# Performance work log

Measured on AMD Instinct MI355X. Metric: run time of the kernel, lower is better.

The kernel has to match this reference:

```python
import jax, jax.numpy as jnp
import numpy as np

B, E, CIN, O = 2, 50000, 8, 128


def _mesh_conv(x, gemm, w, b):
    # MeshCNN MeshConv: x (B,C,E), gemm (B,E,4) neighbor indices, w (O,C,5), b (O,)
    # gather 4 GeMM neighbors per edge, build 5 symmetric features, 1x5 conv
    neigh = jax.vmap(lambda xb, gb: xb[:, gb])(x, gemm)  # (B,C,E,4)
    f1, f2, f3, f4 = neigh[..., 0], neigh[..., 1], neigh[..., 2], neigh[..., 3]
    G = jnp.stack([x, f1 + f3, f2 + f4, jnp.abs(f1 - f3), jnp.abs(f2 - f4)], axis=-1)  # (B,C,E,5)
    return jnp.einsum('bces,ocs->boe', G, w) + b[None, :, None]


def _inorm(x, eps=1e-5):
    # InstanceNorm (no affine, biased variance) over the edge dim, per (batch, channel)
    m = jnp.mean(x, axis=-1, keepdims=True)
    v = jnp.var(x, axis=-1, keepdims=True)
    return (x - m) * jax.lax.rsqrt(v + eps)


def _conv1(x, w, b):
    # 1x1 Conv1d: x (B,C,E), w (O,C)
    return jnp.einsum('bce,oc->boe', x, w) + b[None, :, None]


def setup_inputs() -> dict:
    key = jax.random.key(0)
    ks = jax.random.split(key, 16)

    def W(k, shape, fan):
        return jax.random.normal(k, shape, jnp.float32) * np.float32(1.0 / np.sqrt(fan))

    d = {}
    d['fe'] = jax.random.normal(ks[0], (B, CIN, E), jnp.float32)
    d['gemm'] = jax.random.randint(ks[1], (B, E, 4), 0, E)
    # first-stage MeshConvs: geometry branch (5 ch) and position branch (3 ch)
    d['w_e1'] = W(ks[2], (O, 5, 5), 25);       d['b_e1'] = jnp.zeros((O,), jnp.float32)
    d['w_p1'] = W(ks[3], (O, 3, 5), 15);       d['b_p1'] = jnp.zeros((O,), jnp.float32)
    # residual-block MeshConvs (blocks=1)
    d['w_e2'] = W(ks[4], (O, O, 5), O * 5);    d['b_e2'] = jnp.zeros((O,), jnp.float32)
    d['w_p2'] = W(ks[5], (O, O, 5), O * 5);    d['b_p2'] = jnp.zeros((O,), jnp.float32)
    # Attn(in_dim=O)
    d['wa'] = W(ks[6], (O // 4, O), O);        d['ba'] = jnp.zeros((O // 4,), jnp.float32)
    d['wb'] = W(ks[7], (O // 4, O), O);        d['bb'] = jnp.zeros((O // 4,), jnp.float32)
    d['wal'] = W(ks[8], (O // 2, O // 2), O // 2);  d['bal'] = jnp.zeros((O // 2,), jnp.float32)
    d['wbl'] = W(ks[9], (O // 2, O // 2), O // 2);  d['bbl'] = jnp.zeros((O // 2,), jnp.float32)
    d['wat'] = W(ks[10], (O // 2, O // 2, 5), O // 2 * 5); d['bat'] = jnp.zeros((O // 2,), jnp.float32)
    d['wbt'] = W(ks[11], (O // 2, O // 2, 5), O // 2 * 5); d['bbt'] = jnp.zeros((O // 2,), jnp.float32)
    d['waf'] = W(ks[12], (O, O), O);           d['baf'] = jnp.zeros((O,), jnp.float32)
    d['wbf'] = W(ks[13], (O, O), O);           d['bbf'] = jnp.zeros((O,), jnp.float32)
    return d


def reference(fe, gemm, w_e1, b_e1, w_p1, b_p1, w_e2, b_e2, w_p2, b_p2,
              wa, ba, wb, bb, wal, bal, wbl, bbl, wat, bat, wbt, bbt,
              waf, baf, wbf, bbf):
    # DownConv (8-channel input path): split into edge (5) and point (3) branches
    fe_e, fe_p = fe[:, :5, :], fe[:, 5:, :]
    x1_e = jax.nn.relu(_inorm(_mesh_conv(fe_e, gemm, w_e1, b_e1)))
    x2_e = jax.nn.relu(_inorm(_mesh_conv(x1_e, gemm, w_e2, b_e2)) + x1_e)
    x1_p = jax.nn.relu(_inorm(_mesh_conv(fe_p, gemm, w_p1, b_p1)))
    x2_p = jax.nn.relu(_inorm(_mesh_conv(x1_p, gemm, w_p2, b_p2)) + x1_p)
    # Attn fusion
    x_all = jnp.concatenate([_conv1(x2_e, wa, ba), _conv1(x2_p, wb, bb)], axis=1)  # (B, O/2, E)
    x_a_two = jnp.concatenate([_conv1(x_all, wal, bal), _mesh_conv(x_all, gemm, wat, bat)], axis=1)
    x_b_two = jnp.concatenate([_conv1(x_all, wbl, bbl), _mesh_conv(x_all, gemm, wbt, bbt)], axis=1)
    wA = jax.nn.sigmoid(_inorm(_conv1(x_a_two, waf, baf)))  # (B,O,E)
    wB = jax.nn.sigmoid(_inorm(_conv1(x_b_two, wbf, bbf)))
    weights = jax.nn.softmax(jnp.stack([wA, wB], axis=1), axis=1)  # (B,2,O,E)
    agg = x2_e * weights[:, 0] + x2_p * weights[:, 1]
    # x2_ep = cat(x2_e, x2_p); also emit the attention-fused combine (before_pool)
    return jnp.concatenate([x2_e, x2_p, agg], axis=1)  # (B, 3*O, E)
```

## Files before the change

kernel.cpp:

```cpp
#include <hip/hip_runtime.h>
#include <cstdio>
#include <math.h>


#define E_TOT 50000
#define B_TOT 2
#define TILE_E 64
#define NBLK ((E_TOT + TILE_E - 1) / TILE_E)

typedef _Float16 half_t;
typedef __attribute__((ext_vector_type(4))) _Float16 h4;
typedef __attribute__((ext_vector_type(8))) _Float16 h8;
typedef __attribute__((ext_vector_type(4))) float f32x4;

__device__ __forceinline__ float sigmoidf_(float x) {
    return 1.0f / (1.0f + __expf(-x));
}
__device__ __forceinline__ h8 habs8(h8 x) {
    union { h8 h; unsigned int u[4]; } v;
    v.h = x;
#pragma unroll
    for (int i = 0; i < 4; ++i) v.u[i] &= 0x7FFF7FFFu;
    return v.h;
}

#define OFF_W1E   0
#define OFF_W1P   8192
#define OFF_WTE2  16384
#define OFF_WTP2  98304
#define OFF_WHA   180224
#define OFF_WHB   221184
#define OFF_WTA   262144
#define OFF_WTB   266240
#define OFF_WTAF  270336
#define OFF_WTBF  286720
#define WARENA_N  303104

__global__ __launch_bounds__(256)
void wprep_k(half_t* __restrict__ wa_,
             const float* __restrict__ w_e1, const float* __restrict__ w_p1,
             const float* __restrict__ w_e2, const float* __restrict__ w_p2,
             const float* __restrict__ wat,  const float* __restrict__ wbt,
             const float* __restrict__ wa,   const float* __restrict__ wb,
             const float* __restrict__ wal,  const float* __restrict__ wbl,
             const float* __restrict__ waf,  const float* __restrict__ wbf)
{
    int idx = blockIdx.x * 256 + threadIdx.x;
    switch (blockIdx.y) {
    case 0: if (idx < 8192) { int o = idx >> 6, k = idx & 63, s = k >> 3, cc = k & 7;
            float v = (s < 5 && cc < 5) ? w_e1[o * 25 + cc * 5 + s] : 0.f;
            wa_[OFF_W1E + idx] = (half_t)v; } break;
    case 1: if (idx < 8192) { int o = idx >> 6, k = idx & 63, s = k >> 3, cc = k & 7;
            float v = (s < 5 && cc >= 5) ? w_p1[o * 15 + (cc - 5) * 5 + s] : 0.f;
            wa_[OFF_W1P + idx] = (half_t)v; } break;
    case 2: if (idx < 81920) { int o = idx / 640, r = idx % 640, s = r >> 7, c = r & 127;
            wa_[OFF_WTE2 + idx] = (half_t)w_e2[(o * 128 + c) * 5 + s]; } break;
    case 3: if (idx < 81920) { int o = idx / 640, r = idx % 640, s = r >> 7, c = r & 127;
            wa_[OFF_WTP2 + idx] = (half_t)w_p2[(o * 128 + c) * 5 + s]; } break;
    case 4: if (idx < 40960) { int o = idx / 320, r = idx % 320, s = r >> 6, c = r & 63;
            float v = (o < 64) ? (s == 0 ? wal[o * 64 + c] : 0.f)
                               : wat[((o - 64) * 64 + c) * 5 + s];
            wa_[OFF_WHA + idx] = (half_t)v; } break;
    case 5: if (idx < 40960) { int o = idx / 320, r = idx % 320, s = r >> 6, c = r & 63;
            float v = (o < 64) ? (s == 0 ? wbl[o * 64 + c] : 0.f)
                               : wbt[((o - 64) * 64 + c) * 5 + s];
            wa_[OFF_WHB + idx] = (half_t)v; } break;
    case 6: if (idx < 4096)  wa_[OFF_WTA  + idx] = (half_t)wa[idx];  break;
    case 7: if (idx < 4096)  wa_[OFF_WTB  + idx] = (half_t)wb[idx];  break;
    case 8: if (idx < 16384) wa_[OFF_WTAF + idx] = (half_t)waf[idx]; break;
    case 9: if (idx < 16384) wa_[OFF_WTBF + idx] = (half_t)wbf[idx]; break;
    }
}

__global__ __launch_bounds__(256)
void transpose_in_k(const float* __restrict__ fe, float* __restrict__ fet)
{
    int b = blockIdx.z;
    int e = blockIdx.x * 256 + threadIdx.x;
    if (e >= E_TOT) return;
    float v[8];
#pragma unroll
    for (int c = 0; c < 8; ++c)
        v[c] = fe[((long)b * 8 + c) * E_TOT + e];
    float4* dst = (float4*)&fet[((long)b * E_TOT + e) * 8];
    dst[0] = make_float4(v[0], v[1], v[2], v[3]);
    dst[1] = make_float4(v[4], v[5], v[6], v[7]);
}

__global__ __launch_bounds__(512)
void mesh1_both_k(const float* __restrict__ fet, const int* __restrict__ gemm,
                  const half_t* __restrict__ war,
                  const float* __restrict__ be1, const float* __restrict__ bp1,
                  half_t* __restrict__ tmpe, half_t* __restrict__ tmpp,
                  float* __restrict__ parte, float* __restrict__ partp)
{
    __shared__ h8 Gl[64 * 8];
    __shared__ int nidx[64][4];

    const int tid  = threadIdx.x;
    const int b    = blockIdx.y;
    const int e0   = blockIdx.x * TILE_E;
    const int lane = tid & 63;
    const int wv   = tid >> 6;
    const int l15  = lane & 15;
    const int kg   = lane >> 4;
    const int br   = wv >> 2;
    const int o0   = (wv & 3) * 32;

    const float* xb = fet + (long)b * E_TOT * 8;

    if (tid < 256) {
        int e = tid >> 2, s = tid & 3;
        int eg = e0 + e;
        nidx[e][s] = (eg < E_TOT) ? gemm[((long)b * E_TOT + eg) * 4 + s] : 0;
    }
    __syncthreads();

    {
        int e = tid >> 3, g = tid & 7;
        int eg = e0 + e;
        int se = (eg < E_TOT) ? eg : 0;
        h8 r;
        if (g == 0) {
            const float* p = xb + (long)se * 8;
            float4 v0 = *(const float4*)p, v1 = *(const float4*)(p + 4);
            r[0] = (half_t)v0.x; r[1] = (half_t)v0.y; r[2] = (half_t)v0.z; r[3] = (half_t)v0.w;
            r[4] = (half_t)v1.x; r[5] = (half_t)v1.y; r[6] = (half_t)v1.z; r[7] = (half_t)v1.w;
        } else if (g <= 4) {
            int ia = (g == 1 || g == 3) ? 0 : 1;
            const float* pa = xb + (long)nidx[e][ia] * 8;
            const float* pb = xb + (long)nidx[e][ia + 2] * 8;
            float4 a0 = *(const float4*)pa, a1 = *(const float4*)(pa + 4);
            float4 b0 = *(const float4*)pb, b1 = *(const float4*)(pb + 4);
            float aa[8] = {a0.x, a0.y, a0.z, a0.w, a1.x, a1.y, a1.z, a1.w};
            float bb[8] = {b0.x, b0.y, b0.z, b0.w, b1.x, b1.y, b1.z, b1.w};
            if (g <= 2) {
#pragma unroll
                for (int j = 0; j < 8; ++j) r[j] = (half_t)(aa[j] + bb[j]);
            } else {
#pragma unroll
                for (int j = 0; j < 8; ++j) r[j] = (half_t)fabsf(aa[j] - bb[j]);
            }
        } else {
#pragma unroll
            for (int j = 0; j < 8; ++j) r[j] = (half_t)0.f;
        }
        Gl[(e * 8 + g) ^ (e & 7)] = r;
    }
    __syncthreads();

    f32x4 acc[4][2];
#pragma unroll
    for (int mt = 0; mt < 4; ++mt)
#pragma unroll
        for (int nt = 0; nt < 2; ++nt)
#pragma unroll
            for (int j = 0; j < 4; ++j) acc[mt][nt][j] = 0.f;

    const half_t* wt = war + (br ? OFF_W1P : OFF_W1E);
#pragma unroll
    for (int ks = 0; ks < 2; ++ks) {
        h8 bw[2];
#pragma unroll
        for (int nt = 0; nt < 2; ++nt)
            bw[nt] = *(const h8*)(wt + (long)(o0 + nt * 16 + l15) * 64 + ks * 32 + kg * 8);
#pragma unroll
        for (int mt = 0; mt < 4; ++mt) {
            int row = mt * 16 + l15;
            h8 a = Gl[row * 8 + ((ks * 4 + kg) ^ (row & 7))];
#pragma unroll
            for (int nt = 0; nt < 2; ++nt)
                acc[mt][nt] = __builtin_amdgcn_mfma_f32_16x16x32_f16(a, bw[nt], acc[mt][nt], 0, 0, 0);
        }
    }

    const float* bias = br ? bp1 : be1;
    half_t* yb = (br ? tmpp : tmpe) + (long)b * E_TOT * 128;
    float* part = br ? partp : parte;
    float bv[2], s1[2], s2[2];
#pragma unroll
    for (int nt = 0; nt < 2; ++nt) {
        bv[nt] = bias[o0 + nt * 16 + l15];
        s1[nt] = 0.f; s2[nt] = 0.f;
    }
#pragma unroll
    for (int mt = 0; mt < 4; ++mt) {
        int ebase = e0 + mt * 16 + (kg << 2);
#pragma unroll
        for (int j = 0; j < 4; ++j) {
            if (ebase + j < E_TOT) {
#pragma unroll
                for (int nt = 0; nt < 2; ++nt) {
                    float v = acc[mt][nt][j] + bv[nt];
                    yb[(long)(ebase + j) * 128 + o0 + nt * 16 + l15] = (half_t)v;
                    s1[nt] += v; s2[nt] += v * v;
                }
            }
        }
    }
#pragma unroll
    for (int nt = 0; nt < 2; ++nt) {
        s1[nt] += __shfl_xor(s1[nt], 16); s1[nt] += __shfl_xor(s1[nt], 32);
        s2[nt] += __shfl_xor(s2[nt], 16); s2[nt] += __shfl_xor(s2[nt], 32);
    }
    if (lane < 16) {
        long pb = ((long)b * NBLK + blockIdx.x) * 128;
#pragma unroll
        for (int nt = 0; nt < 2; ++nt) {
            part[(pb + o0 + nt * 16 + lane) * 2 + 0] = s1[nt];
            part[(pb + o0 + nt * 16 + lane) * 2 + 1] = s2[nt];
        }
    }
}

__global__ __launch_bounds__(512, 4)
void mesh2i_k(const half_t* __restrict__ x1i, const int* __restrict__ gemm,
              const half_t* __restrict__ war,
              const float* __restrict__ be, const float* __restrict__ bp,
              half_t* __restrict__ tmpe, half_t* __restrict__ tmpp,
              float* __restrict__ parte, float* __restrict__ partp)
{
    __shared__ h8 B0[1024], B1[1024], B2[1024], B3[1024];
    __shared__ int nidx[64][4];

    const int tid  = threadIdx.x;
    const int b    = blockIdx.y;
    const int e0   = blockIdx.x * TILE_E;
    const int lane = tid & 63;
    const int wv   = tid >> 6;
    const int br   = wv >> 2;
    const int o0   = (wv & 3) * 32;
    const int l15  = lane & 15;
    const int kg   = lane >> 4;

    const half_t* xb = x1i + (long)b * E_TOT * 256;

    if (tid < 256) {
        int e = tid >> 2, s = tid & 3;
        int eg = e0 + e;
        nidx[e][s] = (eg < E_TOT) ? gemm[((long)b * E_TOT + eg) * 4 + s] : 0;
    }
    __syncthreads();

    int te[4], tc[4], tslot[4];
#pragma unroll
    for (int t = 0; t < 4; ++t) {
        int q = t * 512 + tid;
        te[t] = q >> 5; tc[t] = q & 31;
        tslot[t] = (te[t] * 16 + (tc[t] & 15)) ^ (te[t] & 7);
    }

#pragma unroll
    for (int t = 0; t < 4; ++t) {
        int eg = e0 + te[t];
        int se = (eg < E_TOT) ? eg : 0;
        h8 v = *(const h8*)(xb + (long)se * 256 + tc[t] * 8);
        ((tc[t] >> 4) ? B1 : B0)[tslot[t]] = v;
    }
    h8 rA[4], rB[4];
#pragma unroll
    for (int t = 0; t < 4; ++t) {
        int na = nidx[te[t]][0], nb = nidx[te[t]][2];
        rA[t] = *(const h8*)(xb + (long)na * 256 + tc[t] * 8);
        rB[t] = *(const h8*)(xb + (long)nb * 256 + tc[t] * 8);
    }
    __syncthreads();

    f32x4 acc[4][2];
#pragma unroll
    for (int mt = 0; mt < 4; ++mt)
#pragma unroll
        for (int nt = 0; nt < 2; ++nt)
#pragma unroll
            for (int j = 0; j < 4; ++j) acc[mt][nt][j] = 0.f;

    const half_t* wt = war + (br ? OFF_WTP2 : OFF_WTE2);
    auto chunk = [&](const h8* bufE, const h8* bufP, int s) {
        const h8* buf = br ? bufP : bufE;
#pragma unroll
        for (int ks = 0; ks < 4; ++ks) {
            h8 bw0 = *(const h8*)(wt + ((long)(o0 + l15) * 5 + s) * 128 + ks * 32 + kg * 8);
            h8 bw1 = *(const h8*)(wt + ((long)(o0 + 16 + l15) * 5 + s) * 128 + ks * 32 + kg * 8);
#pragma unroll
            for (int mt = 0; mt < 4; ++mt) {
                int row = mt * 16 + l15;
                h8 a = buf[row * 16 + ((ks * 4 + kg) ^ (row & 7))];
                acc[mt][0] = __builtin_amdgcn_mfma_f32_16x16x32_f16(a, bw0, acc[mt][0], 0, 0, 0);
                acc[mt][1] = __builtin_amdgcn_mfma_f32_16x16x32_f16(a, bw1, acc[mt][1], 0, 0, 0);
            }
        }
    };

    chunk(B0, B1, 0);
    __syncthreads();

#pragma unroll
    for (int t = 0; t < 4; ++t) {
        h8 sv = rA[t] + rB[t];
        h8 dv = habs8(rA[t] - rB[t]);
        if (tc[t] >> 4) { B3[tslot[t]] = sv; B1[tslot[t]] = dv; }
        else            { B2[tslot[t]] = sv; B0[tslot[t]] = dv; }
    }
#pragma unroll
    for (int t = 0; t < 4; ++t) {
        int na = nidx[te[t]][1], nb = nidx[te[t]][3];
        rA[t] = *(const h8*)(xb + (long)na * 256 + tc[t] * 8);
        rB[t] = *(const h8*)(xb + (long)nb * 256 + tc[t] * 8);
    }
    __syncthreads();

    chunk(B2, B3, 1);
    chunk(B0, B1, 3);
    __syncthreads();

#pragma unroll
    for (int t = 0; t < 4; ++t) {
        h8 sv = rA[t] + rB[t];
        h8 dv = habs8(rA[t] - rB[t]);
        if (tc[t] >> 4) { B3[tslot[t]] = sv; B1[tslot[t]] = dv; }
        else            { B2[tslot[t]] = sv; B0[tslot[t]] = dv; }
    }
    __syncthreads();

    chunk(B2, B3, 2);
    chunk(B0, B1, 4);

    const float* bias = br ? bp : be;
    half_t* yb = (br ? tmpp : tmpe) + (long)b * E_TOT * 128;
    float* part = br ? partp : parte;
    float bv0 = bias[o0 + l15], bv1 = bias[o0 + 16 + l15];
    float s1a = 0.f, s2a = 0.f, s1b = 0.f, s2b = 0.f;
#pragma unroll
    for (int mt = 0; mt < 4; ++mt) {
        int ebase = e0 + mt * 16 + (kg << 2);
#pragma unroll
        for (int j = 0; j < 4; ++j) {
            if (ebase + j < E_TOT) {
                float v0 = acc[mt][0][j] + bv0;
                float v1 = acc[mt][1][j] + bv1;
                yb[(long)(ebase + j) * 128 + o0 + l15]      = (half_t)v0;
                yb[(long)(ebase + j) * 128 + o0 + 16 + l15] = (half_t)v1;
                s1a += v0; s2a += v0 * v0;
                s1b += v1; s2b += v1 * v1;
            }
        }
    }
    s1a += __shfl_xor(s1a, 16); s1a += __shfl_xor(s1a, 32);
    s2a += __shfl_xor(s2a, 16); s2a += __shfl_xor(s2a, 32);
    s1b += __shfl_xor(s1b, 16); s1b += __shfl_xor(s1b, 32);
    s2b += __shfl_xor(s2b, 16); s2b += __shfl_xor(s2b, 32);
    if (lane < 16) {
        long pb = ((long)b * NBLK + blockIdx.x) * 128;
        part[(pb + o0 + lane) * 2 + 0]      = s1a;
        part[(pb + o0 + lane) * 2 + 1]      = s2a;
        part[(pb + o0 + 16 + lane) * 2 + 0] = s1b;
        part[(pb + o0 + 16 + lane) * 2 + 1] = s2b;
    }
}

__global__ __launch_bounds__(512, 4)
void heads2_k(const half_t* __restrict__ xall, const int* __restrict__ gemm,
              const half_t* __restrict__ war,
              const float* __restrict__ bal, const float* __restrict__ bbl,
              const float* __restrict__ bat, const float* __restrict__ bbt,
              half_t* __restrict__ xa2, half_t* __restrict__ xb2)
{
    __shared__ h8 C0[512], C1[512], C2[512];
    __shared__ int nidx[64][4];

    const int tid  = threadIdx.x;
    const int b    = blockIdx.y;
    const int e0   = blockIdx.x * TILE_E;
    const int lane = tid & 63;
    const int wv   = tid >> 6;
    const int hd   = wv >> 2;
    const int o0   = (wv & 3) * 32;
    const int l15  = lane & 15;
    const int kg   = lane >> 4;

    const half_t* xb = xall + (long)b * E_TOT * 64;

    if (tid < 256) {
        int e = tid >> 2, s = tid & 3;
        int eg = e0 + e;
        nidx[e][s] = (eg < E_TOT) ? gemm[((long)b * E_TOT + eg) * 4 + s] : 0;
    }
    __syncthreads();

    const int te = tid >> 3, tc = tid & 7;
    const int tslot = (te * 8 + tc) ^ (te & 7);

    {
        int eg = e0 + te;
        int se = (eg < E_TOT) ? eg : 0;
        C0[tslot] = *(const h8*)(xb + (long)se * 64 + tc * 8);
    }
    h8 rA, rB;
    {
        int na = nidx[te][0], nb = nidx[te][2];
        rA = *(const h8*)(xb + (long)na * 64 + tc * 8);
        rB = *(const h8*)(xb + (long)nb * 64 + tc * 8);
    }
    __syncthreads();

    f32x4 acc[4][2];
#pragma unroll
    for (int mt = 0; mt < 4; ++mt)
#pragma unroll
        for (int nt = 0; nt < 2; ++nt)
#pragma unroll
            for (int j = 0; j < 4; ++j) acc[mt][nt][j] = 0.f;

    const half_t* wt = war + (hd ? OFF_WHB : OFF_WHA);
    auto chunk = [&](const h8* buf, int s) {
#pragma unroll
        for (int ks = 0; ks < 2; ++ks) {
            h8 bw0 = *(const h8*)(wt + ((long)(o0 + l15) * 5 + s) * 64 + ks * 32 + kg * 8);
            h8 bw1 = *(const h8*)(wt + ((long)(o0 + 16 + l15) * 5 + s) * 64 + ks * 32 + kg * 8);
#pragma unroll
            for (int mt = 0; mt < 4; ++mt) {
                int row = mt * 16 + l15;
                h8 a = buf[row * 8 + ((ks * 4 + kg) ^ (row & 7))];
                acc[mt][0] = __builtin_amdgcn_mfma_f32_16x16x32_f16(a, bw0, acc[mt][0], 0, 0, 0);
                acc[mt][1] = __builtin_amdgcn_mfma_f32_16x16x32_f16(a, bw1, acc[mt][1], 0, 0, 0);
            }
        }
    };

    chunk(C0, 0);
    __syncthreads();
    {
        C1[tslot] = rA + rB;
        C2[tslot] = habs8(rA - rB);
        int na = nidx[te][1], nb = nidx[te][3];
        rA = *(const h8*)(xb + (long)na * 64 + tc * 8);
        rB = *(const h8*)(xb + (long)nb * 64 + tc * 8);
    }
    __syncthreads();
    chunk(C1, 1);
    chunk(C2, 3);
    __syncthreads();
    {
        C1[tslot] = rA + rB;
        C2[tslot] = habs8(rA - rB);
    }
    __syncthreads();
    chunk(C1, 2);
    chunk(C2, 4);

    half_t* yb = (hd ? xb2 : xa2) + (long)b * E_TOT * 128;
    float bv[2];
#pragma unroll
    for (int nt = 0; nt < 2; ++nt) {
        int o = o0 + nt * 16 + l15;
        bv[nt] = (o < 64) ? (hd ? bbl[o] : bal[o]) : (hd ? bbt[o - 64] : bat[o - 64]);
    }
#pragma unroll
    for (int mt = 0; mt < 4; ++mt) {
        int ebase = e0 + mt * 16 + (kg << 2);
#pragma unroll
        for (int j = 0; j < 4; ++j) {
            if (ebase + j < E_TOT) {
#pragma unroll
                for (int nt = 0; nt < 2; ++nt)
                    yb[(long)(ebase + j) * 128 + o0 + nt * 16 + l15] =
                        (half_t)(acc[mt][nt][j] + bv[nt]);
            }
        }
    }
}

__global__ __launch_bounds__(512)
void gates_k(const half_t* __restrict__ xa2, const half_t* __restrict__ xb2,
             const half_t* __restrict__ war,
             const float* __restrict__ baf, const float* __restrict__ bbf,
             half_t* __restrict__ tmpe, half_t* __restrict__ tmpp,
             float* __restrict__ parte, float* __restrict__ partp)
{
    __shared__ h8 Gl[64 * 16];

    const int tid  = threadIdx.x;
    const int br   = blockIdx.y;
    const int b    = blockIdx.z;
    const int e0   = blockIdx.x * TILE_E;
    const int lane = tid & 63;
    const int wv   = tid >> 6;
    const int l15  = lane & 15;
    const int kg   = lane >> 4;
    const int o0   = wv * 16;

    const half_t* xb = (br ? xb2 : xa2) + (long)b * E_TOT * 128;
    const half_t* wt = war + (br ? OFF_WTBF : OFF_WTAF);

#pragma unroll
    for (int t = 0; t < 2; ++t) {
        int q = t * 512 + tid;
        int e = q >> 4, c8 = q & 15;
        int eg = e0 + e;
        int se = (eg < E_TOT) ? eg : 0;
        Gl[(e * 16 + c8) ^ (e & 7)] = *(const h8*)(xb + (long)se * 128 + c8 * 8);
    }
    __syncthreads();

    f32x4 acc[4];
#pragma unroll
    for (int mt = 0; mt < 4; ++mt)
#pragma unroll
        for (int j = 0; j < 4; ++j) acc[mt][j] = 0.f;

#pragma unroll
    for (int ks = 0; ks < 4; ++ks) {
        h8 bw = *(const h8*)(wt + (long)(o0 + l15) * 128 + ks * 32 + kg * 8);
#pragma unroll
        for (int mt = 0; mt < 4; ++mt) {
            int row = mt * 16 + l15;
            h8 a = Gl[row * 16 + ((ks * 4 + kg) ^ (row & 7))];
            acc[mt] = __builtin_amdgcn_mfma_f32_16x16x32_f16(a, bw, acc[mt], 0, 0, 0);
        }
    }

    const float* bias = br ? bbf : baf;
    half_t* yb = (br ? tmpp : tmpe) + (long)b * E_TOT * 128;
    float* part = br ? partp : parte;
    float bv = bias[o0 + l15];
    float s1 = 0.f, s2 = 0.f;
#pragma unroll
    for (int mt = 0; mt < 4; ++mt) {
        int ebase = e0 + mt * 16 + (kg << 2);
#pragma unroll
        for (int j = 0; j < 4; ++j) {
            if (ebase + j < E_TOT) {
                float v = acc[mt][j] + bv;
                yb[(long)(ebase + j) * 128 + o0 + l15] = (half_t)v;
                s1 += v; s2 += v * v;
            }
        }
    }
    s1 += __shfl_xor(s1, 16); s1 += __shfl_xor(s1, 32);
    s2 += __shfl_xor(s2, 16); s2 += __shfl_xor(s2, 32);
    if (lane < 16) {
        long pb = ((long)b * NBLK + blockIdx.x) * 128;
        part[(pb + o0 + lane) * 2 + 0] = s1;
        part[(pb + o0 + lane) * 2 + 1] = s2;
    }
}

__global__ __launch_bounds__(256)
void xall_k(const half_t* __restrict__ x2e, const half_t* __restrict__ x2p,
            const half_t* __restrict__ war,
            const float* __restrict__ ba, const float* __restrict__ bb,
            half_t* __restrict__ xall)
{
    __shared__ h8 Gl[64 * 16];

    const int tid  = threadIdx.x;
    const int br   = blockIdx.y;
    const int b    = blockIdx.z;
    const int e0   = blockIdx.x * TILE_E;
    const int lane = tid & 63;
    const int wv   = tid >> 6;
    const int l15  = lane & 15;
    const int kg   = lane >> 4;
    const int eoff = wv * 16;

    const half_t* xb = (br ? x2p : x2e) + (long)b * E_TOT * 128;
    const half_t* wt = war + (br ? OFF_WTB : OFF_WTA);

#pragma unroll
    for (int t = 0; t < 4; ++t) {
        int q = t * 256 + tid;
        int e = q >> 4, c8 = q & 15;
        int eg = e0 + e;
        int se = (eg < E_TOT) ? eg : 0;
        Gl[(e * 16 + c8) ^ (e & 7)] = *(const h8*)(xb + (long)se * 128 + c8 * 8);
    }
    __syncthreads();

    f32x4 acc[2];
#pragma unroll
    for (int nt = 0; nt < 2; ++nt)
#pragma unroll
        for (int j = 0; j < 4; ++j) acc[nt][j] = 0.f;

#pragma unroll
    for (int ks = 0; ks < 4; ++ks) {
        h8 bw[2];
#pragma unroll
        for (int nt = 0; nt < 2; ++nt)
            bw[nt] = *(const h8*)(wt + (long)(nt * 16 + l15) * 128 + ks * 32 + kg * 8);
        int row = eoff + l15;
        h8 a = Gl[row * 16 + ((ks * 4 + kg) ^ (row & 7))];
#pragma unroll
        for (int nt = 0; nt < 2; ++nt)
            acc[nt] = __builtin_amdgcn_mfma_f32_16x16x32_f16(a, bw[nt], acc[nt], 0, 0, 0);
    }

    const float* bias = br ? bb : ba;
    half_t* yb = xall + (long)b * E_TOT * 64;
    int oOff = br * 32;
#pragma unroll
    for (int nt = 0; nt < 2; ++nt) {
        float bv = bias[nt * 16 + l15];
        int ebase = e0 + eoff + (kg << 2);
#pragma unroll
        for (int j = 0; j < 4; ++j) {
            if (ebase + j < E_TOT)
                yb[(long)(ebase + j) * 64 + oOff + nt * 16 + l15] = (half_t)(acc[nt][j] + bv);
        }
    }
}

__global__ __launch_bounds__(256)
void stats2_k(const float* __restrict__ parte, const float* __restrict__ partp,
              float* __restrict__ statse, float* __restrict__ statsp)
{
    int g = blockIdx.x;
    int br = g >> 8, rem = g & 255, b = rem >> 7, o = rem & 127;
    const float* part = br ? partp : parte;
    float* stats = br ? statsp : statse;
    int tid = threadIdx.x;
    float s1 = 0.f, s2 = 0.f;
    for (int k = tid; k < NBLK; k += 256) {
        long base = (((long)b * NBLK + k) * 128 + o) * 2;
        s1 += part[base];
        s2 += part[base + 1];
    }
#pragma unroll
    for (int d = 1; d < 64; d <<= 1) {
        s1 += __shfl_xor(s1, d);
        s2 += __shfl_xor(s2, d);
    }
    __shared__ float r1[4], r2[4];
    int wv = tid >> 6;
    if ((tid & 63) == 0) { r1[wv] = s1; r2[wv] = s2; }
    __syncthreads();
    if (tid == 0) {
        s1 = r1[0] + r1[1] + r1[2] + r1[3];
        s2 = r2[0] + r2[1] + r2[2] + r2[3];
        float mean = s1 / (float)E_TOT;
        float var  = s2 / (float)E_TOT - mean * mean;
        var = fmaxf(var, 0.f);
        stats[(b * 128 + o) * 2 + 0] = mean;
        stats[(b * 128 + o) * 2 + 1] = rsqrtf(var + 1e-5f);
    }
}

__global__ __launch_bounds__(256)
void norm_act2_k(const half_t* __restrict__ tmpe, const half_t* __restrict__ tmpp,
                 const float* __restrict__ statse, const float* __restrict__ statsp,
                 half_t* __restrict__ x1i)
{
    const long PER = (long)B_TOT * E_TOT * 16;
    long q = (long)blockIdx.x * 256 + threadIdx.x;
    if (q >= 2 * PER) return;
    int br = (q >= PER);
    q -= (long)br * PER;
    const half_t* src = br ? tmpp : tmpe;
    const float* stats = br ? statsp : statse;
    long idx = q * 8;
    int c = (int)(idx & 127);
    long be = idx >> 7;
    int b = (int)(be / E_TOT);
    int e = (int)(be % E_TOT);
    h8 v = *(const h8*)&src[idx];
    h8 r;
#pragma unroll
    for (int j = 0; j < 8; ++j) {
        float2 st = *(const float2*)&stats[(b * 128 + c + j) * 2];
        float t = ((float)v[j] - st.x) * st.y;
        r[j] = (half_t)fmaxf(t, 0.f);
    }
    *(h8*)&x1i[((long)b * E_TOT + e) * 256 + br * 128 + c] = r;
}

__global__ __launch_bounds__(256)
void normres2_k(const half_t* __restrict__ tmpe, const half_t* __restrict__ tmpp,
                const half_t* __restrict__ x1i,
                const float* __restrict__ statse, const float* __restrict__ statsp,
                float* __restrict__ outb,
                half_t* __restrict__ x2e, half_t* __restrict__ x2p)
{
    __shared__ float T[32 * 68];
    int br = blockIdx.y >> 2, cg = blockIdx.y & 3;
    int b = blockIdx.z;
    int e0 = blockIdx.x * 64;
    int tid = threadIdx.x;
    const half_t* xin = br ? tmpp : tmpe;
    const float* stats = br ? statsp : statse;
    half_t* x2b = br ? x2p : x2e;
    int sect = br * 128;
#pragma unroll
    for (int i = 0; i < 2; ++i) {
        int q = tid + i * 256;
        int e = q >> 3, cq = q & 7;
        int eg = e0 + e;
        int se = (eg < E_TOT) ? eg : (E_TOT - 1);
        int c = cg * 32 + cq * 4;
        long base = ((long)b * E_TOT + se) * 128 + c;
        h4 v4 = *(const h4*)&xin[base];
        h4 r4 = *(const h4*)&x1i[((long)b * E_TOT + se) * 256 + br * 128 + c];
        h4 o4;
#pragma unroll
        for (int j = 0; j < 4; ++j) {
            float2 st = *(const float2*)&stats[(b * 128 + c + j) * 2];
            float t = ((float)v4[j] - st.x) * st.y + (float)r4[j];
            t = fmaxf(t, 0.f);
            T[(cq * 4 + j) * 68 + e] = t;
            o4[j] = (half_t)t;
        }
        if (eg < E_TOT) *(h4*)&x2b[base] = o4;
    }
    __syncthreads();
#pragma unroll
    for (int i = 0; i < 2; ++i) {
        int q = tid + i * 256;
        int cl = q >> 4, eq = q & 15;
        int e4 = e0 + eq * 4;
        int cglob = sect + cg * 32 + cl;
        float4 v = *(const float4*)&T[cl * 68 + eq * 4];
        long obase = ((long)b * 384 + cglob) * E_TOT + e4;
        if (e4 + 3 < E_TOT) {
            *(float4*)&outb[obase] = v;
        } else {
            const float* vp = &v.x;
            for (int j = 0; j < 4; ++j)
                if (e4 + j < E_TOT) outb[obase + j] = vp[j];
        }
    }
}

__global__ __launch_bounds__(256)
void gate_agg2_k(const half_t* __restrict__ tA, const half_t* __restrict__ tB,
                 const float* __restrict__ statsA, const float* __restrict__ statsB,
                 const half_t* __restrict__ x2e, const half_t* __restrict__ x2p,
                 float* __restrict__ outb)
{
    __shared__ float T[32 * 68];
    int b = blockIdx.z, cg = blockIdx.y;
    int e0 = blockIdx.x * 64;
    int tid = threadIdx.x;
#pragma unroll
    for (int i = 0; i < 2; ++i) {
        int q = tid + i * 256;
        int e = q >> 3, cq = q & 7;
        int eg = e0 + e;
        int se = (eg < E_TOT) ? eg : (E_TOT - 1);
        int c = cg * 32 + cq * 4;
        long base = ((long)b * E_TOT + se) * 128 + c;
        h4 a4 = *(const h4*)&tA[base];
        h4 b4 = *(const h4*)&tB[base];
        h4 xe4 = *(const h4*)&x2e[base];
        h4 xp4 = *(const h4*)&x2p[base];
#pragma unroll
        for (int j = 0; j < 4; ++j) {
            float2 sa = *(const float2*)&statsA[(b * 128 + c + j) * 2];
            float2 sb = *(const float2*)&statsB[(b * 128 + c + j) * 2];
            float na = sigmoidf_(((float)a4[j] - sa.x) * sa.y);
            float nb = sigmoidf_(((float)b4[j] - sb.x) * sb.y);
            float s = sigmoidf_(na - nb);
            T[(cq * 4 + j) * 68 + e] = (float)xe4[j] * s + (float)xp4[j] * (1.f - s);
        }
    }
    __syncthreads();
#pragma unroll
    for (int i = 0; i < 2; ++i) {
        int q = tid + i * 256;
        int cl = q >> 4, eq = q & 15;
        int e4 = e0 + eq * 4;
        int cglob = cg * 32 + cl;
        float4 v = *(const float4*)&T[cl * 68 + eq * 4];
        long ab = ((long)b * 384 + 256 + cglob) * E_TOT + e4;
        if (e4 + 3 < E_TOT) {
            *(float4*)&outb[ab] = v;
        } else {
            const float* vp = &v.x;
            for (int j = 0; j < 4; ++j)
                if (e4 + j < E_TOT) outb[ab + j] = vp[j];
        }
    }
}

extern "C" void kernel_launch(void* const* d_in, const int* in_sizes, int n_in,
                              void* d_out, int out_size, void* d_ws, size_t ws_size,
                              hipStream_t stream)
{
    const float* fe   = (const float*)d_in[0];
    const int*   gemm = (const int*)  d_in[1];
    const float* w_e1 = (const float*)d_in[2];  const float* b_e1 = (const float*)d_in[3];
    const float* w_p1 = (const float*)d_in[4];  const float* b_p1 = (const float*)d_in[5];
    const float* w_e2 = (const float*)d_in[6];  const float* b_e2 = (const float*)d_in[7];
    const float* w_p2 = (const float*)d_in[8];  const float* b_p2 = (const float*)d_in[9];
    const float* wa   = (const float*)d_in[10]; const float* ba   = (const float*)d_in[11];
    const float* wb   = (const float*)d_in[12]; const float* bb   = (const float*)d_in[13];
    const float* wal  = (const float*)d_in[14]; const float* bal  = (const float*)d_in[15];
    const float* wbl  = (const float*)d_in[16]; const float* bbl  = (const float*)d_in[17];
    const float* wat  = (const float*)d_in[18]; const float* bat  = (const float*)d_in[19];
    const float* wbt  = (const float*)d_in[20]; const float* bbt  = (const float*)d_in[21];
    const float* waf  = (const float*)d_in[22]; const float* baf  = (const float*)d_in[23];
    const float* wbf  = (const float*)d_in[24]; const float* bbf  = (const float*)d_in[25];
    float* out = (float*)d_out;

    const long EB = (long)E_TOT;

    char* wp = (char*)d_ws;
    auto alloc = [&](size_t bytes) -> void* {
        void* r = (void*)wp;
        wp += (bytes + 255) & ~(size_t)255;
        return r;
    };
    float*  FET    = (float*)alloc((size_t)B_TOT * EB * 8 * 4);
    half_t* TMP_E  = (half_t*)alloc((size_t)B_TOT * EB * 128 * 2);
    half_t* TMP_P  = (half_t*)alloc((size_t)B_TOT * EB * 128 * 2);
    half_t* X1I    = (half_t*)alloc((size_t)B_TOT * EB * 256 * 2);
    half_t* X2E    = (half_t*)alloc((size_t)B_TOT * EB * 128 * 2);
    half_t* X2P    = (half_t*)alloc((size_t)B_TOT * EB * 128 * 2);
    half_t* XALL   = (half_t*)alloc((size_t)B_TOT * EB * 64 * 2);
    float*  PART_E = (float*)alloc((size_t)B_TOT * NBLK * 128 * 2 * 4);
    float*  PART_P = (float*)alloc((size_t)B_TOT * NBLK * 128 * 2 * 4);
    float*  STATSE = (float*)alloc((size_t)B_TOT * 128 * 2 * 4);
    float*  STATSP = (float*)alloc((size_t)B_TOT * 128 * 2 * 4);
    half_t* WAR    = (half_t*)alloc((size_t)WARENA_N * 2);

    if ((size_t)(wp - (char*)d_ws) > ws_size) {
        fprintf(stderr, "kernel_launch: ws too small (%zu < %zu)\n",
                ws_size, (size_t)(wp - (char*)d_ws));
        return;
    }

    half_t* XA2 = X1I;
    half_t* XB2 = X1I + (size_t)B_TOT * EB * 128;

    dim3 blk256(256), blk512(512);
    dim3 gI(NBLK, B_TOT);
    dim3 gE2(NBLK, 2, B_TOT);
    dim3 gT((E_TOT + 255) / 256, 1, B_TOT);
    dim3 gN8(NBLK, 8, B_TOT);
    dim3 gN4(NBLK, 4, B_TOT);
    int gA2 = (int)((2 * (long)B_TOT * EB * 16 + 255) / 256);

    wprep_k<<<dim3(320, 10, 1), blk256, 0, stream>>>(WAR,
        w_e1, w_p1, w_e2, w_p2, wat, wbt, wa, wb, wal, wbl, waf, wbf);
    transpose_in_k<<<gT, blk256, 0, stream>>>(fe, FET);

    mesh1_both_k<<<gI, blk512, 0, stream>>>(FET, gemm, WAR, b_e1, b_p1,
        TMP_E, TMP_P, PART_E, PART_P);
    stats2_k<<<512, blk256, 0, stream>>>(PART_E, PART_P, STATSE, STATSP);
    norm_act2_k<<<gA2, blk256, 0, stream>>>(TMP_E, TMP_P, STATSE, STATSP, X1I);

    mesh2i_k<<<gI, blk512, 0, stream>>>(X1I, gemm, WAR, b_e2, b_p2,
        TMP_E, TMP_P, PART_E, PART_P);
    stats2_k<<<512, blk256, 0, stream>>>(PART_E, PART_P, STATSE, STATSP);
    normres2_k<<<gN8, blk256, 0, stream>>>(TMP_E, TMP_P, X1I, STATSE, STATSP,
        out, X2E, X2P);

    xall_k<<<gE2, blk256, 0, stream>>>(X2E, X2P, WAR, ba, bb, XALL);

    heads2_k<<<gI, blk512, 0, stream>>>(XALL, gemm, WAR, bal, bbl, bat, bbt, XA2, XB2);

    gates_k<<<gE2, blk512, 0, stream>>>(XA2, XB2, WAR, baf, bbf,
        TMP_E, TMP_P, PART_E, PART_P);
    stats2_k<<<512, blk256, 0, stream>>>(PART_E, PART_P, STATSE, STATSP);
    gate_agg2_k<<<gN4, blk256, 0, stream>>>(TMP_E, TMP_P, STATSE, STATSP,
        X2E, X2P, out);
}
```

Before: 375.7 us.

## Split interleaved X1 buffer and run branch-separate mesh conv blocks

Replaces the interleaved 256-channel X1 layout with separate edge and point buffers, and launches the second mesh conv with one branch per block (grid dimension y). Each block now gathers only its own branch's 128 channels, rather than loading both branches and letting each half of the waves use one. Waves now each compute 16 output channels rather than 32. The change also halves shared memory per block and drops the 4-blocks occupancy hint, aiming for more resident blocks and less wasted gather traffic. The cost is that neighbor indices and the tile setup are now done twice per edge tile.

```diff
diff --git a/kernel.cpp b/kernel.cpp
--- a/kernel.cpp
+++ b/kernel.cpp
@@ -213,27 +213,29 @@
     }
 }
 
-__global__ __launch_bounds__(512, 4)
-void mesh2i_k(const half_t* __restrict__ x1i, const int* __restrict__ gemm,
-              const half_t* __restrict__ war,
+__global__ __launch_bounds__(512)
+void mesh2p_k(const half_t* __restrict__ x1e, const half_t* __restrict__ x1p,
+              const int* __restrict__ gemm, const half_t* __restrict__ war,
               const float* __restrict__ be, const float* __restrict__ bp,
               half_t* __restrict__ tmpe, half_t* __restrict__ tmpp,
               float* __restrict__ parte, float* __restrict__ partp)
 {
-    __shared__ h8 B0[1024], B1[1024], B2[1024], B3[1024];
+    __shared__ h8 A[1024];
+    __shared__ h8 Bs[1024];
     __shared__ int nidx[64][4];
 
     const int tid  = threadIdx.x;
-    const int b    = blockIdx.y;
+    const int br   = blockIdx.y;
+    const int b    = blockIdx.z;
     const int e0   = blockIdx.x * TILE_E;
     const int lane = tid & 63;
     const int wv   = tid >> 6;
-    const int br   = wv >> 2;
-    const int o0   = (wv & 3) * 32;
     const int l15  = lane & 15;
     const int kg   = lane >> 4;
-
-    const half_t* xb = x1i + (long)b * E_TOT * 256;
+    const int o0   = wv * 16;
+
+    const half_t* xb = (br ? x1p : x1e) + (long)b * E_TOT * 128;
+    const half_t* wt = war + (br ? OFF_WTP2 : OFF_WTE2);
 
     if (tid < 256) {
         int e = tid >> 2, s = tid & 3;
@@ -242,123 +244,103 @@
     }
     __syncthreads();
 
-    int te[4], tc[4], tslot[4];
-#pragma unroll
-    for (int t = 0; t < 4; ++t) {
+    int te[2], tc[2], ts[2];
+#pragma unroll
+    for (int t = 0; t < 2; ++t) {
         int q = t * 512 + tid;
-        te[t] = q >> 5; tc[t] = q & 31;
-        tslot[t] = (te[t] * 16 + (tc[t] & 15)) ^ (te[t] & 7);
-    }
-
-#pragma unroll
-    for (int t = 0; t < 4; ++t) {
+        te[t] = q >> 4; tc[t] = q & 15;
+        ts[t] = (te[t] * 16 + tc[t]) ^ (te[t] & 7);
+    }
+
+#pragma unroll
+    for (int t = 0; t < 2; ++t) {
         int eg = e0 + te[t];
         int se = (eg < E_TOT) ? eg : 0;
-        h8 v = *(const h8*)(xb + (long)se * 256 + tc[t] * 8);
-        ((tc[t] >> 4) ? B1 : B0)[tslot[t]] = v;
-    }
-    h8 rA[4], rB[4];
-#pragma unroll
-    for (int t = 0; t < 4; ++t) {
-        int na = nidx[te[t]][0], nb = nidx[te[t]][2];
-        rA[t] = *(const h8*)(xb + (long)na * 256 + tc[t] * 8);
-        rB[t] = *(const h8*)(xb + (long)nb * 256 + tc[t] * 8);
-    }
-    __syncthreads();
-
-    f32x4 acc[4][2];
+        A[ts[t]] = *(const h8*)(xb + (long)se * 128 + tc[t] * 8);
+    }
+    h8 rA[2], rB[2];
+#pragma unroll
+    for (int t = 0; t < 2; ++t) {
+        rA[t] = *(const h8*)(xb + (long)nidx[te[t]][0] * 128 + tc[t] * 8);
+        rB[t] = *(const h8*)(xb + (long)nidx[te[t]][2] * 128 + tc[t] * 8);
+    }
+    __syncthreads();
+
+    f32x4 acc[4];
 #pragma unroll
     for (int mt = 0; mt < 4; ++mt)
 #pragma unroll
-        for (int nt = 0; nt < 2; ++nt)
-#pragma unroll
-            for (int j = 0; j < 4; ++j) acc[mt][nt][j] = 0.f;
-
-    const half_t* wt = war + (br ? OFF_WTP2 : OFF_WTE2);
-    auto chunk = [&](const h8* bufE, const h8* bufP, int s) {
-        const h8* buf = br ? bufP : bufE;
+        for (int j = 0; j < 4; ++j) acc[mt][j] = 0.f;
+
+    auto chunk = [&](const h8* buf, int s) {
 #pragma unroll
         for (int ks = 0; ks < 4; ++ks) {
-            h8 bw0 = *(const h8*)(wt + ((long)(o0 + l15) * 5 + s) * 128 + ks * 32 + kg * 8);
-            h8 bw1 = *(const h8*)(wt + ((long)(o0 + 16 + l15) * 5 + s) * 128 + ks * 32 + kg * 8);
+            h8 bw = *(const h8*)(wt + ((long)(o0 + l15) * 5 + s) * 128 + ks * 32 + kg * 8);
 #pragma unroll
             for (int mt = 0; mt < 4; ++mt) {
                 int row = mt * 16 + l15;
                 h8 a = buf[row * 16 + ((ks * 4 + kg) ^ (row & 7))];
-                acc[mt][0] = __builtin_amdgcn_mfma_f32_16x16x32_f16(a, bw0, acc[mt][0], 0, 0, 0);
-                acc[mt][1] = __builtin_amdgcn_mfma_f32_16x16x32_f16(a, bw1, acc[mt][1], 0, 0, 0);
+                acc[mt] = __builtin_amdgcn_mfma_f32_16x16x32_f16(a, bw, acc[mt], 0, 0, 0);
             }
         }
     };
 
-    chunk(B0, B1, 0);
-    __syncthreads();
-
-#pragma unroll
-    for (int t = 0; t < 4; ++t) {
-        h8 sv = rA[t] + rB[t];
-        h8 dv = habs8(rA[t] - rB[t]);
-        if (tc[t] >> 4) { B3[tslot[t]] = sv; B1[tslot[t]] = dv; }
-        else            { B2[tslot[t]] = sv; B0[tslot[t]] = dv; }
-    }
-#pragma unroll
-    for (int t = 0; t < 4; ++t) {
-        int na = nidx[te[t]][1], nb = nidx[te[t]][3];
-        rA[t] = *(const h8*)(xb + (long)na * 256 + tc[t] * 8);
-        rB[t] = *(const h8*)(xb + (long)nb * 256 + tc[t] * 8);
-    }
-    __syncthreads();
-
-    chunk(B2, B3, 1);
-    chunk(B0, B1, 3);
-    __syncthreads();
-
-#pragma unroll
-    for (int t = 0; t < 4; ++t) {
-        h8 sv = rA[t] + rB[t];
-        h8 dv = habs8(rA[t] - rB[t]);
-        if (tc[t] >> 4) { B3[tslot[t]] = sv; B1[tslot[t]] = dv; }
-        else            { B2[tslot[t]] = sv; B0[tslot[t]] = dv; }
-    }
-    __syncthreads();
-
-    chunk(B2, B3, 2);
-    chunk(B0, B1, 4);
+    chunk(A, 0);
+    __syncthreads();
+
+#pragma unroll
+    for (int t = 0; t < 2; ++t) {
+        Bs[ts[t]] = rA[t] + rB[t];
+        A[ts[t]]  = habs8(rA[t] - rB[t]);
+    }
+#pragma unroll
+    for (int t = 0; t < 2; ++t) {
+        rA[t] = *(const h8*)(xb + (long)nidx[te[t]][1] * 128 + tc[t] * 8);
+        rB[t] = *(const h8*)(xb + (long)nidx[te[t]][3] * 128 + tc[t] * 8);
+    }
+    __syncthreads();
+
+    chunk(Bs, 1);
+    chunk(A, 3);
+    __syncthreads();
+
+#pragma unroll
+    for (int t = 0; t < 2; ++t) {
+        Bs[ts[t]] = rA[t] + rB[t];
+        A[ts[t]]  = habs8(rA[t] - rB[t]);
+    }
+    __syncthreads();
+
+    chunk(Bs, 2);
+    chunk(A, 4);
 
     const float* bias = br ? bp : be;
     half_t* yb = (br ? tmpp : tmpe) + (long)b * E_TOT * 128;
     float* part = br ? partp : parte;
-    float bv0 = bias[o0 + l15], bv1 = bias[o0 + 16 + l15];
-    float s1a = 0.f, s2a = 0.f, s1b = 0.f, s2b = 0.f;
+    float bv = bias[o0 + l15];
+    float s1 = 0.f, s2 = 0.f;
 #pragma unroll
     for (int mt = 0; mt < 4; ++mt) {
         int ebase = e0 + mt * 16 + (kg << 2);
 #pragma unroll
         for (int j = 0; j < 4; ++j) {
             if (ebase + j < E_TOT) {
-                float v0 = acc[mt][0][j] + bv0;
-                float v1 = acc[mt][1][j] + bv1;
-                yb[(long)(ebase + j) * 128 + o0 + l15]      = (half_t)v0;
-                yb[(long)(ebase + j) * 128 + o0 + 16 + l15] = (half_t)v1;
-                s1a += v0; s2a += v0 * v0;
-                s1b += v1; s2b += v1 * v1;
+                float v = acc[mt][j] + bv;
+                yb[(long)(ebase + j) * 128 + o0 + l15] = (half_t)v;
+                s1 += v; s2 += v * v;
             }
         }
     }
-    s1a += __shfl_xor(s1a, 16); s1a += __shfl_xor(s1a, 32);
-    s2a += __shfl_xor(s2a, 16); s2a += __shfl_xor(s2a, 32);
-    s1b += __shfl_xor(s1b, 16); s1b += __shfl_xor(s1b, 32);
-    s2b += __shfl_xor(s2b, 16); s2b += __shfl_xor(s2b, 32);
+    s1 += __shfl_xor(s1, 16); s1 += __shfl_xor(s1, 32);
+    s2 += __shfl_xor(s2, 16); s2 += __shfl_xor(s2, 32);
     if (lane < 16) {
         long pb = ((long)b * NBLK + blockIdx.x) * 128;
-        part[(pb + o0 + lane) * 2 + 0]      = s1a;
-        part[(pb + o0 + lane) * 2 + 1]      = s2a;
-        part[(pb + o0 + 16 + lane) * 2 + 0] = s1b;
-        part[(pb + o0 + 16 + lane) * 2 + 1] = s2b;
-    }
-}
-
-__global__ __launch_bounds__(512, 4)
+        part[(pb + o0 + lane) * 2 + 0] = s1;
+        part[(pb + o0 + lane) * 2 + 1] = s2;
+    }
+}
+
+__global__ __launch_bounds__(512)
 void heads2_k(const half_t* __restrict__ xall, const int* __restrict__ gemm,
               const half_t* __restrict__ war,
               const float* __restrict__ bal, const float* __restrict__ bbl,
@@ -648,7 +630,7 @@
 __global__ __launch_bounds__(256)
 void norm_act2_k(const half_t* __restrict__ tmpe, const half_t* __restrict__ tmpp,
                  const float* __restrict__ statse, const float* __restrict__ statsp,
-                 half_t* __restrict__ x1i)
+                 half_t* __restrict__ x1e, half_t* __restrict__ x1p)
 {
     const long PER = (long)B_TOT * E_TOT * 16;
     long q = (long)blockIdx.x * 256 + threadIdx.x;
@@ -657,11 +639,10 @@
     q -= (long)br * PER;
     const half_t* src = br ? tmpp : tmpe;
     const float* stats = br ? statsp : statse;
+    half_t* dst = br ? x1p : x1e;
     long idx = q * 8;
     int c = (int)(idx & 127);
-    long be = idx >> 7;
-    int b = (int)(be / E_TOT);
-    int e = (int)(be % E_TOT);
+    int b = (int)((idx >> 7) / E_TOT);
     h8 v = *(const h8*)&src[idx];
     h8 r;
 #pragma unroll
@@ -670,12 +651,12 @@
         float t = ((float)v[j] - st.x) * st.y;
         r[j] = (half_t)fmaxf(t, 0.f);
     }
-    *(h8*)&x1i[((long)b * E_TOT + e) * 256 + br * 128 + c] = r;
+    *(h8*)&dst[idx] = r;
 }
 
 __global__ __launch_bounds__(256)
 void normres2_k(const half_t* __restrict__ tmpe, const half_t* __restrict__ tmpp,
-                const half_t* __restrict__ x1i,
+                const half_t* __restrict__ x1e, const half_t* __restrict__ x1p,
                 const float* __restrict__ statse, const float* __restrict__ statsp,
                 float* __restrict__ outb,
                 half_t* __restrict__ x2e, half_t* __restrict__ x2p)
@@ -686,6 +667,7 @@
     int e0 = blockIdx.x * 64;
     int tid = threadIdx.x;
     const half_t* xin = br ? tmpp : tmpe;
+    const half_t* res = br ? x1p : x1e;
     const float* stats = br ? statsp : statse;
     half_t* x2b = br ? x2p : x2e;
     int sect = br * 128;
@@ -698,7 +680,7 @@
         int c = cg * 32 + cq * 4;
         long base = ((long)b * E_TOT + se) * 128 + c;
         h4 v4 = *(const h4*)&xin[base];
-        h4 r4 = *(const h4*)&x1i[((long)b * E_TOT + se) * 256 + br * 128 + c];
+        h4 r4 = *(const h4*)&res[base];
         h4 o4;
 #pragma unroll
         for (int j = 0; j < 4; ++j) {
@@ -811,7 +793,8 @@
     float*  FET    = (float*)alloc((size_t)B_TOT * EB * 8 * 4);
     half_t* TMP_E  = (half_t*)alloc((size_t)B_TOT * EB * 128 * 2);
     half_t* TMP_P  = (half_t*)alloc((size_t)B_TOT * EB * 128 * 2);
-    half_t* X1I    = (half_t*)alloc((size_t)B_TOT * EB * 256 * 2);
+    half_t* X1E    = (half_t*)alloc((size_t)B_TOT * EB * 128 * 2);
+    half_t* X1P    = (half_t*)alloc((size_t)B_TOT * EB * 128 * 2);
     half_t* X2E    = (half_t*)alloc((size_t)B_TOT * EB * 128 * 2);
     half_t* X2P    = (half_t*)alloc((size_t)B_TOT * EB * 128 * 2);
     half_t* XALL   = (half_t*)alloc((size_t)B_TOT * EB * 64 * 2);
@@ -827,8 +810,8 @@
         return;
     }
 
-    half_t* XA2 = X1I;
-    half_t* XB2 = X1I + (size_t)B_TOT * EB * 128;
+    half_t* XA2 = X1E;
+    half_t* XB2 = X1P;
 
     dim3 blk256(256), blk512(512);
     dim3 gI(NBLK, B_TOT);
@@ -845,12 +828,12 @@
     mesh1_both_k<<<gI, blk512, 0, stream>>>(FET, gemm, WAR, b_e1, b_p1,
         TMP_E, TMP_P, PART_E, PART_P);
     stats2_k<<<512, blk256, 0, stream>>>(PART_E, PART_P, STATSE, STATSP);
-    norm_act2_k<<<gA2, blk256, 0, stream>>>(TMP_E, TMP_P, STATSE, STATSP, X1I);
-
-    mesh2i_k<<<gI, blk512, 0, stream>>>(X1I, gemm, WAR, b_e2, b_p2,
+    norm_act2_k<<<gA2, blk256, 0, stream>>>(TMP_E, TMP_P, STATSE, STATSP, X1E, X1P);
+
+    mesh2p_k<<<gE2, blk512, 0, stream>>>(X1E, X1P, gemm, WAR, b_e2, b_p2,
         TMP_E, TMP_P, PART_E, PART_P);
     stats2_k<<<512, blk256, 0, stream>>>(PART_E, PART_P, STATSE, STATSP);
-    normres2_k<<<gN8, blk256, 0, stream>>>(TMP_E, TMP_P, X1I, STATSE, STATSP,
+    normres2_k<<<gN8, blk256, 0, stream>>>(TMP_E, TMP_P, X1E, X1P, STATSE, STATSP,
         out, X2E, X2P);
 
     xall_k<<<gE2, blk256, 0, stream>>>(X2E, X2P, WAR, ba, bb, XALL);
```

Measured after the change: 370.4 us. Within noise of the previous version (-1.4%).
